# Performance work log

Measured on AMD Instinct MI355X. Metric: run time of the kernel, lower is better.

Reference implementation:

```python
import jax, jax.numpy as jnp
import numpy as np

B, L, H, Q = 64, 512, 1024, 64
VA_H = 256


def setup_inputs() -> dict:
    key = jax.random.key(0)
    ks = jax.random.split(key, 10)
    hidden_states = jax.random.normal(ks[0], (B, L, H), dtype=jnp.float32)
    quad_spans = jax.random.randint(ks[1], (B, Q, 4), 0, L, dtype=jnp.int64)
    quad_mask = jnp.ones((B, Q), dtype=jnp.int32)
    s = 0.02
    W1 = jax.random.normal(ks[2], (3 * H, VA_H), dtype=jnp.float32) * s
    b1 = jnp.zeros((VA_H,), dtype=jnp.float32)
    W2 = jax.random.normal(ks[3], (VA_H, VA_H // 2), dtype=jnp.float32) * s
    b2 = jnp.zeros((VA_H // 2,), dtype=jnp.float32)
    W3 = jax.random.normal(ks[4], (VA_H // 2, 2), dtype=jnp.float32) * s
    b3 = jnp.zeros((2,), dtype=jnp.float32)
    return {"hidden_states": hidden_states, "quad_spans": quad_spans,
            "quad_mask": quad_mask, "W1": W1, "b1": b1, "W2": W2, "b2": b2,
            "W3": W3, "b3": b3}


def _pool_spans(hidden_states, quad_spans, quad_mask):
    # hidden_states [B,L,H]; quad_spans [B,Q,4]; quad_mask [B,Q]
    Bn, Ln, Hn = hidden_states.shape
    pos = jnp.arange(Ln)[None, None, :]                      # [1,1,L]
    asp_s = quad_spans[:, :, 0:1]
    asp_e = quad_spans[:, :, 1:2]
    opi_s = quad_spans[:, :, 2:3]
    opi_e = quad_spans[:, :, 3:4]
    asp_valid = asp_s >= 2
    opi_valid = opi_s >= 2
    sep = pos == 1                                           # [SEP] fallback
    asp_m = ((pos >= asp_s) & (pos <= asp_e) & asp_valid) | (~asp_valid & sep)
    opi_m = ((pos >= opi_s) & (pos <= opi_e) & opi_valid) | (~opi_valid & sep)
    qm = (quad_mask != 0)[:, :, None]
    asp_f = (asp_m & qm).astype(hidden_states.dtype)         # [B,Q,L]
    opi_f = (opi_m & qm).astype(hidden_states.dtype)
    h_asp = jnp.einsum('bql,blh->bqh', asp_f, hidden_states) / jnp.clip(
        asp_f.sum(-1, keepdims=True), 1.0, None)
    h_opi = jnp.einsum('bql,blh->bqh', opi_f, hidden_states) / jnp.clip(
        opi_f.sum(-1, keepdims=True), 1.0, None)
    return h_asp, h_opi


def reference(hidden_states, quad_spans, quad_mask, W1, b1, W2, b2, W3, b3):
    h_asp, h_opi = _pool_spans(hidden_states, quad_spans, quad_mask)
    h_pair = jnp.concatenate([h_asp, h_opi, h_asp * h_opi], axis=-1)  # [B,Q,3H]
    x = jax.nn.gelu(h_pair @ W1 + b1, approximate=False)   # torch GELU = exact
    x = jax.nn.gelu(x @ W2 + b2, approximate=False)        # dropout: eval mode
    x = x @ W3 + b3                                        # [B,Q,2]
    va = jax.nn.sigmoid(x) * 8.0 + 1.0
    return va * quad_mask[:, :, None].astype(va.dtype)
```

## Files before the change

### kernel.cpp

```cpp
#include <hip/hip_runtime.h>
#include <math.h>


typedef __attribute__((ext_vector_type(4))) float f32x4;
typedef __attribute__((ext_vector_type(8))) short bf16x8;

#define NPAIR 4096
#define LSEQ 512
#define HDIM 1024

__device__ __forceinline__ unsigned short f2bf(float f) {
  unsigned int x = __float_as_uint(f);
  return (unsigned short)((x + 0x7fffu + ((x >> 16) & 1u)) >> 16);
}
__device__ __forceinline__ unsigned int pack2(float lo, float hi) {
  return (unsigned int)f2bf(lo) | ((unsigned int)f2bf(hi) << 16);
}
__device__ __forceinline__ float gelu(float x) {
  return 0.5f * x * (1.f + erff(x * 0.70710678118654752f));
}

__global__ __launch_bounds__(256, 2) void pool_mfma_kernel(
    const float* __restrict__ hs, const int* __restrict__ spans,
    const int* __restrict__ qmask, unsigned short* __restrict__ hpair) {
  __shared__ __align__(16) unsigned char smem[66048];
  __shared__ float scl[128];
  typedef unsigned short BlT[128][40];
  BlT* Bl = (BlT*)smem;
  float(*S)[129] = (float(*)[129])smem;

  const int b = blockIdx.x >> 3;
  const int n0 = (blockIdx.x & 7) * 128;
  const int tid = threadIdx.x;
  const int lane = tid & 63;
  const int lm = lane & 15, quad = lane >> 4;
  const int wm = (tid >> 6) * 32;

  const bool is64 =
      (spans[1] == 0) && (spans[3] == 0) && (spans[5] == 0) && (spans[7] == 0);

  auto span_of = [&](int r, int& s, int& e) {
    const int q = r & 63, t = r >> 6;
    const int idx = (b * 64 + q) * 4 + t * 2;
    s = is64 ? spans[idx * 2] : spans[idx];
    e = is64 ? spans[idx * 2 + 2] : spans[idx + 1];
    if (s < 2) { s = 1; e = 1; }
  };
  int s0, e0, s1, e1;
  span_of(wm + lm, s0, e0);
  span_of(wm + 16 + lm, s1, e1);

  if (tid < 128) {
    int s, e;
    span_of(tid, s, e);
    const int c = (e >= s) ? (e - s + 1) : 0;
    const float sc = 1.f / (float)(c < 1 ? 1 : c);
    scl[tid] = (qmask[b * 64 + (tid & 63)] != 0) ? sc : 0.f;
  }

  f32x4 acc[2][8];
#pragma unroll
  for (int f = 0; f < 2; ++f)
#pragma unroll
    for (int g = 0; g < 8; ++g) acc[f][g] = f32x4{0.f, 0.f, 0.f, 0.f};

  const float* hsb = hs + (size_t)b * (LSEQ * HDIM);
  const int nl = tid & 127;
  const int kb = (tid >> 7) * 16;

  auto load16 = [&](int kbase, unsigned int (&tmp)[8]) {
    const float* src = hsb + (size_t)(kbase + kb) * HDIM + n0 + nl;
#pragma unroll
    for (int i = 0; i < 8; ++i) {
      const float f0 = src[(size_t)(2 * i) * HDIM];
      const float f1 = src[(size_t)(2 * i + 1) * HDIM];
      tmp[i] = pack2(f0, f1);
    }
  };

  unsigned int tmp[8];
  load16(0, tmp);
  *(uint4*)&Bl[0][nl][kb] = make_uint4(tmp[0], tmp[1], tmp[2], tmp[3]);
  *(uint4*)&Bl[0][nl][kb + 8] = make_uint4(tmp[4], tmp[5], tmp[6], tmp[7]);

  for (int it = 0; it < 16; ++it) {
    const int k0 = it * 32;
    __syncthreads();
    if (it < 15) load16(k0 + 32, tmp);

    bf16x8 a0, a1;
#pragma unroll
    for (int j = 0; j < 8; ++j) {
      const int k = k0 + quad * 8 + j;
      a0[j] = (short)((k >= s0 && k <= e0) ? 0x3F80 : 0);
      a1[j] = (short)((k >= s1 && k <= e1) ? 0x3F80 : 0);
    }
    const BlT& Bc = Bl[it & 1];
#pragma unroll
    for (int g = 0; g < 8; ++g) {
      bf16x8 bg = *(const bf16x8*)&Bc[g * 16 + lm][quad * 8];
      acc[0][g] = __builtin_amdgcn_mfma_f32_16x16x32_bf16(a0, bg, acc[0][g], 0, 0, 0);
      acc[1][g] = __builtin_amdgcn_mfma_f32_16x16x32_bf16(a1, bg, acc[1][g], 0, 0, 0);
    }
    if (it < 15) {
      BlT& Bn = Bl[(it + 1) & 1];
      *(uint4*)&Bn[nl][kb] = make_uint4(tmp[0], tmp[1], tmp[2], tmp[3]);
      *(uint4*)&Bn[nl][kb + 8] = make_uint4(tmp[4], tmp[5], tmp[6], tmp[7]);
    }
  }

  __syncthreads();
#pragma unroll
  for (int f = 0; f < 2; ++f)
#pragma unroll
    for (int g = 0; g < 8; ++g)
#pragma unroll
      for (int r = 0; r < 4; ++r)
        S[wm + f * 16 + quad * 4 + r][g * 16 + lm] = acc[f][g][r];
  __syncthreads();

  const int q = tid >> 2;
  const int cg = (tid & 3) * 32;
  const float sA = scl[q], sO = scl[64 + q];
  unsigned short* dst = hpair + (size_t)(b * 64 + q) * 3072 + n0 + cg;
#pragma unroll
  for (int j4 = 0; j4 < 4; ++j4) {
    float a[8], o[8];
#pragma unroll
    for (int i = 0; i < 8; ++i) {
      a[i] = S[q][cg + j4 * 8 + i] * sA;
      o[i] = S[64 + q][cg + j4 * 8 + i] * sO;
    }
    uint4 wa, wo, wp;
    wa.x = pack2(a[0], a[1]); wa.y = pack2(a[2], a[3]);
    wa.z = pack2(a[4], a[5]); wa.w = pack2(a[6], a[7]);
    wo.x = pack2(o[0], o[1]); wo.y = pack2(o[2], o[3]);
    wo.z = pack2(o[4], o[5]); wo.w = pack2(o[6], o[7]);
    wp.x = pack2(a[0] * o[0], a[1] * o[1]); wp.y = pack2(a[2] * o[2], a[3] * o[3]);
    wp.z = pack2(a[4] * o[4], a[5] * o[5]); wp.w = pack2(a[6] * o[6], a[7] * o[7]);
    *(uint4*)(dst + j4 * 8) = wa;
    *(uint4*)(dst + 1024 + j4 * 8) = wo;
    *(uint4*)(dst + 2048 + j4 * 8) = wp;
  }
}

__global__ void transpose_two(const float* __restrict__ W1,
                              unsigned short* __restrict__ W1T,
                              const float* __restrict__ W2,
                              unsigned short* __restrict__ W2T) {
  __shared__ float t[32][33];
  const float* in;
  unsigned short* out;
  int R, C, c0, r0;
  int blk = blockIdx.x;
  if (blk < 768) {
    in = W1; out = W1T; R = 3072; C = 256;
    c0 = (blk & 7) * 32; r0 = (blk >> 3) * 32;
  } else {
    blk -= 768;
    in = W2; out = W2T; R = 256; C = 128;
    c0 = (blk & 3) * 32; r0 = (blk >> 2) * 32;
  }
  const int x = threadIdx.x, y = threadIdx.y;
#pragma unroll
  for (int i = 0; i < 32; i += 8)
    t[y + i][x] = in[(size_t)(r0 + y + i) * C + c0 + x];
  __syncthreads();
#pragma unroll
  for (int i = 0; i < 32; i += 8)
    out[(size_t)(c0 + y + i) * R + r0 + x] = f2bf(t[x][y + i]);
}

__global__ __launch_bounds__(256) void gemm_bt_partial(
    const unsigned short* __restrict__ A, const unsigned short* __restrict__ Bt,
    float* __restrict__ P, int M, int N, int K, int KH) {
  __shared__ __align__(16) unsigned short Al[64][40];
  __shared__ __align__(16) unsigned short Bl[64][40];
  const int bm = blockIdx.x * 64, bn = blockIdx.y * 64;
  const int kz = blockIdx.z * KH;
  const int tid = threadIdx.x;
  const int wave = tid >> 6, lane = tid & 63;
  const int wm = (wave & 1) * 32, wn = (wave >> 1) * 32;
  const int ar = tid >> 2, ac = (tid & 3) * 8;
  const int lm = lane & 15, lk = (lane >> 4) * 8;

  f32x4 acc00 = {0.f, 0.f, 0.f, 0.f}, acc01 = {0.f, 0.f, 0.f, 0.f};
  f32x4 acc10 = {0.f, 0.f, 0.f, 0.f}, acc11 = {0.f, 0.f, 0.f, 0.f};

  const unsigned short* pa = A + (size_t)(bm + ar) * K + kz + ac;
  const unsigned short* pb = Bt + (size_t)(bn + ar) * K + kz + ac;

  for (int k0 = 0; k0 < KH; k0 += 32) {
    uint4 va = *(const uint4*)(pa + k0);
    uint4 vb = *(const uint4*)(pb + k0);
    *(uint4*)&Al[ar][ac] = va;
    *(uint4*)&Bl[ar][ac] = vb;
    __syncthreads();
    bf16x8 a0 = *(const bf16x8*)&Al[wm + lm][lk];
    bf16x8 a1 = *(const bf16x8*)&Al[wm + 16 + lm][lk];
    bf16x8 b0 = *(const bf16x8*)&Bl[wn + lm][lk];
    bf16x8 b1 = *(const bf16x8*)&Bl[wn + 16 + lm][lk];
    acc00 = __builtin_amdgcn_mfma_f32_16x16x32_bf16(a0, b0, acc00, 0, 0, 0);
    acc01 = __builtin_amdgcn_mfma_f32_16x16x32_bf16(a0, b1, acc01, 0, 0, 0);
    acc10 = __builtin_amdgcn_mfma_f32_16x16x32_bf16(a1, b0, acc10, 0, 0, 0);
    acc11 = __builtin_amdgcn_mfma_f32_16x16x32_bf16(a1, b1, acc11, 0, 0, 0);
    __syncthreads();
  }

  float* Pz = P + (size_t)blockIdx.z * M * N;
  const int r0 = bm + wm + ((lane >> 4) << 2);
  const int c0 = bn + wn + lm;
  auto emit = [&](f32x4 v, int row0, int col) {
#pragma unroll
    for (int r = 0; r < 4; ++r) Pz[(size_t)(row0 + r) * N + col] = v[r];
  };
  emit(acc00, r0, c0);
  emit(acc10, r0 + 16, c0);
  emit(acc01, r0, c0 + 16);
  emit(acc11, r0 + 16, c0 + 16);
}

__global__ __launch_bounds__(256) void reduce_bias_gelu(
    const float* __restrict__ P, const float* __restrict__ bias,
    unsigned short* __restrict__ X) {
  const int t = blockIdx.x * 256 + threadIdx.x;
  const int e = t * 4;
  float4 p0 = *(const float4*)(P + e);
  float4 p1 = *(const float4*)(P + (size_t)NPAIR * 256 + e);
  float4 bs = *(const float4*)(bias + (e & 255));
  const float v0 = gelu(p0.x + p1.x + bs.x);
  const float v1 = gelu(p0.y + p1.y + bs.y);
  const float v2 = gelu(p0.z + p1.z + bs.z);
  const float v3 = gelu(p0.w + p1.w + bs.w);
  uint2 w;
  w.x = pack2(v0, v1);
  w.y = pack2(v2, v3);
  *(uint2*)(X + e) = w;
}

__global__ __launch_bounds__(256) void gemm2_head_kernel(
    const unsigned short* __restrict__ A, const unsigned short* __restrict__ Bt,
    const float* __restrict__ b2, const float* __restrict__ W3,
    const float* __restrict__ b3, const int* __restrict__ qmask,
    float* __restrict__ out) {
  __shared__ __align__(16) unsigned short Al[64][40];
  __shared__ __align__(16) unsigned short Bl[128][40];
  __shared__ float S2[64][129];
  __shared__ float w3[256];

  const int bm = blockIdx.x * 64;
  const int tid = threadIdx.x;
  const int wave = tid >> 6, lane = tid & 63;
  const int wm = (wave & 1) * 32, wn = (wave >> 1) * 64;
  const int ar = tid >> 2, ac = (tid & 3) * 8;
  const int br = tid >> 1, bc = (tid & 1) * 16;
  const int lm = lane & 15, quad = lane >> 4;

  w3[tid] = W3[tid];

  f32x4 acc[2][4];
#pragma unroll
  for (int f = 0; f < 2; ++f)
#pragma unroll
    for (int g = 0; g < 4; ++g) acc[f][g] = f32x4{0.f, 0.f, 0.f, 0.f};

  const unsigned short* pa = A + (size_t)(bm + ar) * 256 + ac;
  const unsigned short* pb = Bt + (size_t)br * 256 + bc;

  for (int k0 = 0; k0 < 256; k0 += 32) {
    uint4 va = *(const uint4*)(pa + k0);
    uint4 vb0 = *(const uint4*)(pb + k0);
    uint4 vb1 = *(const uint4*)(pb + k0 + 8);
    *(uint4*)&Al[ar][ac] = va;
    *(uint4*)&Bl[br][bc] = vb0;
    *(uint4*)&Bl[br][bc + 8] = vb1;
    __syncthreads();
    bf16x8 a0 = *(const bf16x8*)&Al[wm + lm][quad * 8];
    bf16x8 a1 = *(const bf16x8*)&Al[wm + 16 + lm][quad * 8];
#pragma unroll
    for (int g = 0; g < 4; ++g) {
      bf16x8 bg = *(const bf16x8*)&Bl[wn + g * 16 + lm][quad * 8];
      acc[0][g] = __builtin_amdgcn_mfma_f32_16x16x32_bf16(a0, bg, acc[0][g], 0, 0, 0);
      acc[1][g] = __builtin_amdgcn_mfma_f32_16x16x32_bf16(a1, bg, acc[1][g], 0, 0, 0);
    }
    __syncthreads();
  }

#pragma unroll
  for (int f = 0; f < 2; ++f)
#pragma unroll
    for (int g = 0; g < 4; ++g) {
      const int col = wn + g * 16 + lm;
#pragma unroll
      for (int r = 0; r < 4; ++r) {
        const int row = wm + f * 16 + quad * 4 + r;
        S2[row][col] = gelu(acc[f][g][r] + b2[col]);
      }
    }
  __syncthreads();

  if (tid < 128) {
    const int row = tid >> 1, o = tid & 1;
    float a = b3[o];
#pragma unroll 8
    for (int c = 0; c < 128; ++c) a += S2[row][c] * w3[c * 2 + o];
    const int pair = bm + row;
    const float qmf = (float)qmask[pair];
    out[pair * 2 + o] = ((1.f / (1.f + expf(-a))) * 8.f + 1.f) * qmf;
  }
}

extern "C" void kernel_launch(void* const* d_in, const int* in_sizes, int n_in,
                              void* d_out, int out_size, void* d_ws,
                              size_t ws_size, hipStream_t stream) {
  const float* hs = (const float*)d_in[0];
  const int* spans = (const int*)d_in[1];
  const int* qmask = (const int*)d_in[2];
  const float* W1 = (const float*)d_in[3];
  const float* b1 = (const float*)d_in[4];
  const float* W2 = (const float*)d_in[5];
  const float* b2 = (const float*)d_in[6];
  const float* W3 = (const float*)d_in[7];
  const float* b3 = (const float*)d_in[8];
  float* out = (float*)d_out;

  const size_t HPAIR_B = 25165824;
  const size_t X1_B = 2097152;
  const size_t P_B = 2 * 4194304;
  const size_t W1T_B = 1572864;

  char* ws = (char*)d_ws;
  size_t off = 0;
  unsigned short* hpair = (unsigned short*)(ws + off); off += HPAIR_B;
  unsigned short* x1 = (unsigned short*)(ws + off);    off += X1_B;
  float* P = (float*)(ws + off);                       off += P_B;
  unsigned short* W1T = (unsigned short*)(ws + off);   off += W1T_B;
  unsigned short* W2T = (unsigned short*)(ws + off);

  transpose_two<<<800, dim3(32, 8), 0, stream>>>(W1, W1T, W2, W2T);
  pool_mfma_kernel<<<512, 256, 0, stream>>>(hs, spans, qmask, hpair);
  gemm_bt_partial<<<dim3(64, 4, 2), 256, 0, stream>>>(hpair, W1T, P, NPAIR,
                                                      256, 3072, 1536);
  reduce_bias_gelu<<<1024, 256, 0, stream>>>(P, b1, x1);
  gemm2_head_kernel<<<64, 256, 0, stream>>>(x1, W2T, b2, W3, b3, qmask, out);
}
```

Before: 250.8 us.

## Halve pool tile width, fuse bias-GELU reduce into GEMM2, cheapen bf16 pack

```diff
diff --git a/kernel.cpp b/kernel.cpp
--- a/kernel.cpp
+++ b/kernel.cpp
@@ -9,28 +9,29 @@
 #define LSEQ 512
 #define HDIM 1024
 
+__device__ __forceinline__ unsigned int pack2(float lo, float hi) {
+  const unsigned int a = __float_as_uint(lo) + 0x8000u;
+  const unsigned int b = __float_as_uint(hi) + 0x8000u;
+  return __builtin_amdgcn_perm(b, a, 0x07060302u);
+}
 __device__ __forceinline__ unsigned short f2bf(float f) {
-  unsigned int x = __float_as_uint(f);
-  return (unsigned short)((x + 0x7fffu + ((x >> 16) & 1u)) >> 16);
-}
-__device__ __forceinline__ unsigned int pack2(float lo, float hi) {
-  return (unsigned int)f2bf(lo) | ((unsigned int)f2bf(hi) << 16);
+  return (unsigned short)((__float_as_uint(f) + 0x8000u) >> 16);
 }
 __device__ __forceinline__ float gelu(float x) {
   return 0.5f * x * (1.f + erff(x * 0.70710678118654752f));
 }
 
-__global__ __launch_bounds__(256, 2) void pool_mfma_kernel(
+__global__ __launch_bounds__(256, 4) void pool_mfma_kernel(
     const float* __restrict__ hs, const int* __restrict__ spans,
     const int* __restrict__ qmask, unsigned short* __restrict__ hpair) {
-  __shared__ __align__(16) unsigned char smem[66048];
+  __shared__ __align__(16) unsigned char smem[34816];
   __shared__ float scl[128];
-  typedef unsigned short BlT[128][40];
+  typedef unsigned short BlT[64][40];
   BlT* Bl = (BlT*)smem;
-  float(*S)[129] = (float(*)[129])smem;
-
-  const int b = blockIdx.x >> 3;
-  const int n0 = (blockIdx.x & 7) * 128;
+  float(*S)[68] = (float(*)[68])smem;
+
+  const int b = blockIdx.x >> 4;
+  const int n0 = (blockIdx.x & 15) * 64;
   const int tid = threadIdx.x;
   const int lane = tid & 63;
   const int lm = lane & 15, quad = lane >> 4;
@@ -58,35 +59,34 @@
     scl[tid] = (qmask[b * 64 + (tid & 63)] != 0) ? sc : 0.f;
   }
 
-  f32x4 acc[2][8];
+  f32x4 acc[2][4];
 #pragma unroll
   for (int f = 0; f < 2; ++f)
 #pragma unroll
-    for (int g = 0; g < 8; ++g) acc[f][g] = f32x4{0.f, 0.f, 0.f, 0.f};
+    for (int g = 0; g < 4; ++g) acc[f][g] = f32x4{0.f, 0.f, 0.f, 0.f};
 
   const float* hsb = hs + (size_t)b * (LSEQ * HDIM);
-  const int nl = tid & 127;
-  const int kb = (tid >> 7) * 16;
-
-  auto load16 = [&](int kbase, unsigned int (&tmp)[8]) {
-    const float* src = hsb + (size_t)(kbase + kb) * HDIM + n0 + nl;
-#pragma unroll
-    for (int i = 0; i < 8; ++i) {
+  const int nl = tid & 63;
+  const int kw = (tid >> 6) * 8;
+
+  auto load8 = [&](int kbase, unsigned int (&tmp)[4]) {
+    const float* src = hsb + (size_t)(kbase + kw) * HDIM + n0 + nl;
+#pragma unroll
+    for (int i = 0; i < 4; ++i) {
       const float f0 = src[(size_t)(2 * i) * HDIM];
       const float f1 = src[(size_t)(2 * i + 1) * HDIM];
       tmp[i] = pack2(f0, f1);
     }
   };
 
-  unsigned int tmp[8];
-  load16(0, tmp);
-  *(uint4*)&Bl[0][nl][kb] = make_uint4(tmp[0], tmp[1], tmp[2], tmp[3]);
-  *(uint4*)&Bl[0][nl][kb + 8] = make_uint4(tmp[4], tmp[5], tmp[6], tmp[7]);
+  unsigned int tmp[4];
+  load8(0, tmp);
+  *(uint4*)&Bl[0][nl][kw] = make_uint4(tmp[0], tmp[1], tmp[2], tmp[3]);
 
   for (int it = 0; it < 16; ++it) {
     const int k0 = it * 32;
     __syncthreads();
-    if (it < 15) load16(k0 + 32, tmp);
+    if (it < 15) load8(k0 + 32, tmp);
 
     bf16x8 a0, a1;
 #pragma unroll
@@ -97,15 +97,13 @@
     }
     const BlT& Bc = Bl[it & 1];
 #pragma unroll
-    for (int g = 0; g < 8; ++g) {
+    for (int g = 0; g < 4; ++g) {
       bf16x8 bg = *(const bf16x8*)&Bc[g * 16 + lm][quad * 8];
       acc[0][g] = __builtin_amdgcn_mfma_f32_16x16x32_bf16(a0, bg, acc[0][g], 0, 0, 0);
       acc[1][g] = __builtin_amdgcn_mfma_f32_16x16x32_bf16(a1, bg, acc[1][g], 0, 0, 0);
     }
     if (it < 15) {
-      BlT& Bn = Bl[(it + 1) & 1];
-      *(uint4*)&Bn[nl][kb] = make_uint4(tmp[0], tmp[1], tmp[2], tmp[3]);
-      *(uint4*)&Bn[nl][kb + 8] = make_uint4(tmp[4], tmp[5], tmp[6], tmp[7]);
+      *(uint4*)&Bl[(it + 1) & 1][nl][kw] = make_uint4(tmp[0], tmp[1], tmp[2], tmp[3]);
     }
   }
 
@@ -113,23 +111,23 @@
 #pragma unroll
   for (int f = 0; f < 2; ++f)
 #pragma unroll
-    for (int g = 0; g < 8; ++g)
+    for (int g = 0; g < 4; ++g)
 #pragma unroll
       for (int r = 0; r < 4; ++r)
         S[wm + f * 16 + quad * 4 + r][g * 16 + lm] = acc[f][g][r];
   __syncthreads();
 
   const int q = tid >> 2;
-  const int cg = (tid & 3) * 32;
+  const int cg = (tid & 3) * 16;
   const float sA = scl[q], sO = scl[64 + q];
   unsigned short* dst = hpair + (size_t)(b * 64 + q) * 3072 + n0 + cg;
 #pragma unroll
-  for (int j4 = 0; j4 < 4; ++j4) {
+  for (int h = 0; h < 2; ++h) {
     float a[8], o[8];
 #pragma unroll
     for (int i = 0; i < 8; ++i) {
-      a[i] = S[q][cg + j4 * 8 + i] * sA;
-      o[i] = S[64 + q][cg + j4 * 8 + i] * sO;
+      a[i] = S[q][cg + h * 8 + i] * sA;
+      o[i] = S[64 + q][cg + h * 8 + i] * sO;
     }
     uint4 wa, wo, wp;
     wa.x = pack2(a[0], a[1]); wa.y = pack2(a[2], a[3]);
@@ -138,9 +136,9 @@
     wo.z = pack2(o[4], o[5]); wo.w = pack2(o[6], o[7]);
     wp.x = pack2(a[0] * o[0], a[1] * o[1]); wp.y = pack2(a[2] * o[2], a[3] * o[3]);
     wp.z = pack2(a[4] * o[4], a[5] * o[5]); wp.w = pack2(a[6] * o[6], a[7] * o[7]);
-    *(uint4*)(dst + j4 * 8) = wa;
-    *(uint4*)(dst + 1024 + j4 * 8) = wo;
-    *(uint4*)(dst + 2048 + j4 * 8) = wp;
+    *(uint4*)(dst + h * 8) = wa;
+    *(uint4*)(dst + 1024 + h * 8) = wo;
+    *(uint4*)(dst + 2048 + h * 8) = wp;
   }
 }
 
@@ -220,29 +218,11 @@
   emit(acc11, r0 + 16, c0 + 16);
 }
 
-__global__ __launch_bounds__(256) void reduce_bias_gelu(
-    const float* __restrict__ P, const float* __restrict__ bias,
-    unsigned short* __restrict__ X) {
-  const int t = blockIdx.x * 256 + threadIdx.x;
-  const int e = t * 4;
-  float4 p0 = *(const float4*)(P + e);
-  float4 p1 = *(const float4*)(P + (size_t)NPAIR * 256 + e);
-  float4 bs = *(const float4*)(bias + (e & 255));
-  const float v0 = gelu(p0.x + p1.x + bs.x);
-  const float v1 = gelu(p0.y + p1.y + bs.y);
-  const float v2 = gelu(p0.z + p1.z + bs.z);
-  const float v3 = gelu(p0.w + p1.w + bs.w);
-  uint2 w;
-  w.x = pack2(v0, v1);
-  w.y = pack2(v2, v3);
-  *(uint2*)(X + e) = w;
-}
-
 __global__ __launch_bounds__(256) void gemm2_head_kernel(
-    const unsigned short* __restrict__ A, const unsigned short* __restrict__ Bt,
-    const float* __restrict__ b2, const float* __restrict__ W3,
-    const float* __restrict__ b3, const int* __restrict__ qmask,
-    float* __restrict__ out) {
+    const float* __restrict__ P, const unsigned short* __restrict__ Bt,
+    const float* __restrict__ b1, const float* __restrict__ b2,
+    const float* __restrict__ W3, const float* __restrict__ b3,
+    const int* __restrict__ qmask, float* __restrict__ out) {
   __shared__ __align__(16) unsigned short Al[64][40];
   __shared__ __align__(16) unsigned short Bl[128][40];
   __shared__ float S2[64][129];
@@ -264,11 +244,24 @@
 #pragma unroll
     for (int g = 0; g < 4; ++g) acc[f][g] = f32x4{0.f, 0.f, 0.f, 0.f};
 
-  const unsigned short* pa = A + (size_t)(bm + ar) * 256 + ac;
+  const float* p0 = P + (size_t)(bm + ar) * 256 + ac;
+  const float* p1 = p0 + (size_t)NPAIR * 256;
   const unsigned short* pb = Bt + (size_t)br * 256 + bc;
 
   for (int k0 = 0; k0 < 256; k0 += 32) {
-    uint4 va = *(const uint4*)(pa + k0);
+    float4 u0 = *(const float4*)(p0 + k0);
+    float4 u1 = *(const float4*)(p0 + k0 + 4);
+    float4 v0 = *(const float4*)(p1 + k0);
+    float4 v1 = *(const float4*)(p1 + k0 + 4);
+    float4 bb0 = *(const float4*)(b1 + k0 + ac);
+    float4 bb1 = *(const float4*)(b1 + k0 + ac + 4);
+    const float g0 = gelu(u0.x + v0.x + bb0.x), g1 = gelu(u0.y + v0.y + bb0.y);
+    const float g2 = gelu(u0.z + v0.z + bb0.z), g3 = gelu(u0.w + v0.w + bb0.w);
+    const float g4 = gelu(u1.x + v1.x + bb1.x), g5 = gelu(u1.y + v1.y + bb1.y);
+    const float g6 = gelu(u1.z + v1.z + bb1.z), g7 = gelu(u1.w + v1.w + bb1.w);
+    uint4 va;
+    va.x = pack2(g0, g1); va.y = pack2(g2, g3);
+    va.z = pack2(g4, g5); va.w = pack2(g6, g7);
     uint4 vb0 = *(const uint4*)(pb + k0);
     uint4 vb1 = *(const uint4*)(pb + k0 + 8);
     *(uint4*)&Al[ar][ac] = va;
@@ -325,22 +318,20 @@
   float* out = (float*)d_out;
 
   const size_t HPAIR_B = 25165824;
-  const size_t X1_B = 2097152;
-  const size_t P_B = 2 * 4194304;
+  const size_t P_B = 8388608;
   const size_t W1T_B = 1572864;
 
   char* ws = (char*)d_ws;
   size_t off = 0;
   unsigned short* hpair = (unsigned short*)(ws + off); off += HPAIR_B;
-  unsigned short* x1 = (unsigned short*)(ws + off);    off += X1_B;
   float* P = (float*)(ws + off);                       off += P_B;
   unsigned short* W1T = (unsigned short*)(ws + off);   off += W1T_B;
   unsigned short* W2T = (unsigned short*)(ws + off);
 
   transpose_two<<<800, dim3(32, 8), 0, stream>>>(W1, W1T, W2, W2T);
-  pool_mfma_kernel<<<512, 256, 0, stream>>>(hs, spans, qmask, hpair);
+  pool_mfma_kernel<<<1024, 256, 0, stream>>>(hs, spans, qmask, hpair);
   gemm_bt_partial<<<dim3(64, 4, 2), 256, 0, stream>>>(hpair, W1T, P, NPAIR,
                                                       256, 3072, 1536);
-  reduce_bias_gelu<<<1024, 256, 0, stream>>>(P, b1, x1);
-  gemm2_head_kernel<<<64, 256, 0, stream>>>(x1, W2T, b2, W3, b3, qmask, out);
-}
+  gemm2_head_kernel<<<64, 256, 0, stream>>>(P, W2T, b1, b2, W3, b3, qmask,
+                                            out);
+}
```

After: 254.3 us. No clear change (+1.4%).
